# Performance work log

Hardware: AMD Instinct MI355X
Metric: run time of the kernel (lower is better)

Reference implementation:

```python
import jax, jax.numpy as jnp
import numpy as np

NUM_HEADS = 4
INITIAL_VALUE = 1.0
HEADS_RANGE = 3.0


def rotate_every_two(x):
    x1 = x[..., ::2]
    x2 = x[..., 1::2]
    return jnp.stack([-x2, x1], axis=-1).reshape(x.shape)


def theta_shift(x, sin, cos):
    return x * cos + rotate_every_two(x) * sin


def rel_pos_2d(h, w, key_dim):
    # angle: repeat each frequency twice -> length key_dim
    base = 1.0 / 10000.0 ** jnp.linspace(0.0, 1.0, key_dim // 2)
    angle = jnp.repeat(base, 2)
    decay = jnp.log(1.0 - 2.0 ** (-(INITIAL_VALUE + HEADS_RANGE * jnp.arange(NUM_HEADS, dtype=jnp.float32) / NUM_HEADS)))
    idx = jnp.arange(h * w, dtype=jnp.float32)
    sin = jnp.sin(idx[:, None] * angle[None, :]).reshape(h, w, key_dim)
    cos = jnp.cos(idx[:, None] * angle[None, :]).reshape(h, w, key_dim)
    def decay_1d(l):
        i = jnp.arange(l, dtype=jnp.float32)
        return jnp.abs(i[:, None] - i[None, :])[None, :, :] * decay[:, None, None]  # (n, l, l)
    return sin, cos, decay_1d(h), decay_1d(w)


def setup_inputs() -> dict:
    key = jax.random.key(0)
    b, C, H, W = 16, 256, 64, 64
    ks = jax.random.split(key, 12)
    gain = 2.0 ** (-2.5)
    xav = (2.0 / (C + C)) ** 0.5
    return {
        "x": jax.random.normal(ks[0], (b, C, H, W), jnp.float32),
        "Wq": jax.random.normal(ks[1], (C, C), jnp.float32) * gain * xav,
        "bq": jnp.zeros((C,), jnp.float32),
        "Wk": jax.random.normal(ks[2], (C, C), jnp.float32) * gain * xav,
        "bk": jnp.zeros((C,), jnp.float32),
        "Wv": jax.random.normal(ks[3], (C, C), jnp.float32) * gain * xav,
        "bv": jnp.zeros((C,), jnp.float32),
        "dw_kernel": jax.random.normal(ks[4], (5, 5, 1, C), jnp.float32) * 0.05,
        "dw_bias": jnp.zeros((C,), jnp.float32),
        "Wo": jax.random.normal(ks[5], (C, C), jnp.float32) * xav,
        "bo": jnp.zeros((C,), jnp.float32),
    }


def reference(x, Wq, bq, Wk, bk, Wv, bv, dw_kernel, dw_bias, Wo, bo):
    x = jnp.transpose(x, (0, 2, 3, 1))  # (b, h, w, c)
    b, h, w, c = x.shape
    n = NUM_HEADS
    d = c // n  # key_dim == head_dim (value_factor=1)
    scaling = d ** (-0.5)

    sin, cos, mask_h, mask_w = rel_pos_2d(h, w, d)

    q = x @ Wq + bq
    k = (x @ Wk + bk) * scaling
    v = x @ Wv + bv  # (b, h, w, c)

    # depthwise 5x5 conv (lepe) on v, NHWC
    lepe = jax.lax.conv_general_dilated(
        v, dw_kernel, window_strides=(1, 1), padding=((2, 2), (2, 2)),
        dimension_numbers=("NHWC", "HWIO", "NHWC"), feature_group_count=c,
    ) + dw_bias

    q = q.reshape(b, h, w, n, d).transpose(0, 3, 1, 2, 4)  # (b, n, h, w, d)
    k = k.reshape(b, h, w, n, d).transpose(0, 3, 1, 2, 4)
    qr = theta_shift(q, sin, cos)  # sin/cos (h,w,d) broadcast
    kr = theta_shift(k, sin, cos)

    # width-axis attention: rows independent
    qr_w = qr.transpose(0, 2, 1, 3, 4)  # (b, h, n, w, d)
    kr_w = kr.transpose(0, 2, 1, 3, 4)
    v5 = v.reshape(b, h, w, n, d).transpose(0, 1, 3, 2, 4)  # (b, h, n, w, d)
    qk_w = jnp.einsum("bhnqd,bhnkd->bhnqk", qr_w, kr_w) + mask_w  # (b,h,n,w,w)
    v5 = jnp.einsum("bhnqk,bhnkd->bhnqd", jax.nn.softmax(qk_w, axis=-1), v5)

    # height-axis attention: columns independent
    qr_h = qr.transpose(0, 3, 1, 2, 4)  # (b, w, n, h, d)
    kr_h = kr.transpose(0, 3, 1, 2, 4)
    v6 = v5.transpose(0, 3, 2, 1, 4)  # (b, w, n, h, d)
    qk_h = jnp.einsum("bwnqd,bwnkd->bwnqk", qr_h, kr_h) + mask_h  # (b,w,n,h,h)
    out = jnp.einsum("bwnqk,bwnkd->bwnqd", jax.nn.softmax(qk_h, axis=-1), v6)

    out = out.transpose(0, 3, 1, 2, 4).reshape(b, h, w, c)  # (b,h,w,n*d)
    out = (out + lepe) @ Wo + bo
    return jnp.transpose(out, (0, 3, 1, 2))  # (b, c, h, w)
```

## Files before the change

kernel.cpp:

```cpp
#include <hip/hip_runtime.h>
#include <hip/hip_bf16.h>

typedef unsigned short u16;
typedef unsigned int   u32;
typedef __attribute__((ext_vector_type(8))) short bf16x8;
typedef __attribute__((ext_vector_type(4))) float f32x4;

__device__ __forceinline__ float bf2f(u16 u) {
    union { u32 i; float f; } x; x.i = ((u32)u) << 16; return x.f;
}
__device__ __forceinline__ u16 f2bf(float f) {
    union { float f; u32 i; } x; x.f = f;
    u32 i = x.i;
    u32 r = (i + 0x7fffu + ((i >> 16) & 1u)) >> 16;
    return (u16)r;
}

__global__ void k_tables(float2* __restrict__ csT) {
    int id = blockIdx.x * 256 + threadIdx.x;
    int t = id >> 5, i = id & 31;
    double ang = pow(10000.0, -(double)i / 31.0);
    double a = (double)t * ang;
    csT[id] = make_float2((float)cos(a), (float)sin(a));
}

__global__ __launch_bounds__(256) void k_prep_w(
    const float* __restrict__ Wq, const float* __restrict__ Wk,
    const float* __restrict__ Wv, const float* __restrict__ Wo,
    u16* __restrict__ WTq, u16* __restrict__ WTk,
    u16* __restrict__ WTv, u16* __restrict__ WoT)
{
    __shared__ float T[32][33];
    int z = blockIdx.z;
    const float* W = (z == 0) ? Wq : (z == 1) ? Wk : (z == 2) ? Wv : Wo;
    u16* WT        = (z == 0) ? WTq : (z == 1) ? WTk : (z == 2) ? WTv : WoT;
    int n0 = blockIdx.x * 32, k0 = blockIdx.y * 32;
    int tx = threadIdx.x & 31, ty = threadIdx.x >> 5;
#pragma unroll
    for (int i = 0; i < 4; i++)
        T[ty * 4 + i][tx] = W[(k0 + ty * 4 + i) * 256 + n0 + tx];
    __syncthreads();
#pragma unroll
    for (int i = 0; i < 4; i++)
        WT[(n0 + ty * 4 + i) * 256 + k0 + tx] = f2bf(T[tx][ty * 4 + i]);
}

__global__ __launch_bounds__(512, 1) void k_qkv_fused(
    const float* __restrict__ x, const u16* __restrict__ WTall,
    const float* __restrict__ bq, const float* __restrict__ bk,
    const float* __restrict__ bv,
    const float2* __restrict__ csT,
    u16* __restrict__ qr, u16* __restrict__ kr, u16* __restrict__ vO)
{
    __shared__ alignas(16) u16 Alds[128 * 256];
    __shared__ alignas(16) u16 Blds[2][256 * 64];
    __shared__ float2 SL[128 * 32];

    const int tid = threadIdx.x;
    const int t0 = blockIdx.x * 128;
    const int br = tid >> 3, bc = tid & 7;

    bf16x8 breg[4];
#pragma unroll
    for (int p = 0; p < 4; ++p)
        breg[p] = *(const bf16x8*)(WTall + (size_t)(p * 64 + br) * 256 + bc * 8);

    {
        float* Bf = (float*)&Blds[0][0];
        const int b0 = t0 >> 12, sb0 = t0 & 4095;
        const float* xb = x + ((size_t)b0 * 256) * 4096 + sb0;
#pragma unroll
        for (int ch = 0; ch < 2; ++ch) {
#pragma unroll
            for (int p = 0; p < 8; ++p) {
                int it = p * 512 + tid;
                int c = it >> 5, s4 = (it & 31) * 4;
                float4 v4 = *(const float4*)(xb + (size_t)(ch * 128 + c) * 4096 + s4);
                *(float4*)(Bf + c * 128 + s4) = v4;
            }
            __syncthreads();
#pragma unroll
            for (int p = 0; p < 4; ++p) {
                int it = p * 512 + tid;
                int tok = it & 127, ck = it >> 7;
                u16 tmp[8];
#pragma unroll
                for (int j = 0; j < 8; ++j)
                    tmp[j] = f2bf(Bf[(ck * 8 + j) * 128 + tok]);
                int gc = ch * 16 + ck;
                int gcs = (gc & 24) | ((gc & 7) ^ (tok & 7));
                *(bf16x8*)(Alds + tok * 256 + gcs * 8) = *(bf16x8*)tmp;
            }
            __syncthreads();
        }
    }

    {
        const int sb = t0 & 4095;
#pragma unroll
        for (int p = 0; p < 8; ++p) {
            int idx = p * 512 + tid;
            SL[idx] = csT[(size_t)sb * 32 + idx];
        }
    }

    const int lane = tid & 63, w = tid >> 6;
    const int wr = w >> 2, wc = w & 3;
    const int l15 = lane & 15, l4 = lane >> 4, l7 = lane & 7;

#pragma unroll
    for (int mat = 0; mat < 3; ++mat) {
        f32x4 acc[4][4];
#pragma unroll
        for (int mi = 0; mi < 4; ++mi)
#pragma unroll
            for (int ni = 0; ni < 4; ++ni) acc[mi][ni] = (f32x4)0.f;

#pragma unroll
        for (int ks = 0; ks < 4; ++ks) {
            const int s = mat * 4 + ks;
            u16* Bl = &Blds[s & 1][0];
#pragma unroll
            for (int p = 0; p < 4; ++p) {
                int r = p * 64 + br;
                *(bf16x8*)(Bl + r * 64 + (bc ^ (r & 7)) * 8) = breg[p];
            }
            __syncthreads();
            if (s < 11) {
                const int s2 = s + 1;
                const int mat2 = s2 >> 2, ks2 = s2 & 3;
#pragma unroll
                for (int p = 0; p < 4; ++p)
                    breg[p] = *(const bf16x8*)(WTall + (size_t)mat2 * 65536 +
                                (size_t)(p * 64 + br) * 256 + ks2 * 64 + bc * 8);
            }
#pragma unroll
            for (int kk = 0; kk < 2; ++kk) {
                bf16x8 af[4], bfr[4];
#pragma unroll
                for (int mi = 0; mi < 4; ++mi) {
                    int r = wr * 64 + mi * 16 + l15;
                    af[mi] = *(const bf16x8*)(Alds + r * 256 + (ks * 8 + ((kk * 4 + l4) ^ l7)) * 8);
                }
#pragma unroll
                for (int ni = 0; ni < 4; ++ni) {
                    int r = wc * 64 + ni * 16 + l15;
                    bfr[ni] = *(const bf16x8*)(Bl + r * 64 + ((kk * 4 + l4) ^ l7) * 8);
                }
#pragma unroll
                for (int mi = 0; mi < 4; ++mi)
#pragma unroll
                    for (int ni = 0; ni < 4; ++ni)
                        acc[mi][ni] = __builtin_amdgcn_mfma_f32_16x16x32_bf16(
                            af[mi], bfr[ni], acc[mi][ni], 0, 0, 0);
            }
        }

        const float* bias = (mat == 0) ? bq : (mat == 1) ? bk : bv;
        u16* out          = (mat == 0) ? qr : (mat == 1) ? kr : vO;
        const float kscale = (mat == 1) ? 0.125f : 1.0f;
        float bcol[4]; int ip[4];
#pragma unroll
        for (int ni = 0; ni < 4; ++ni) {
            bcol[ni] = bias[wc * 64 + ni * 16 + l15];
            ip[ni] = (ni * 16 + l15) >> 1;
        }
#pragma unroll
        for (int mi = 0; mi < 4; ++mi) {
#pragma unroll
            for (int rg = 0; rg < 4; ++rg) {
                const int sl = wr * 64 + mi * 16 + l4 * 4 + rg;
                size_t trow = (size_t)(t0 + sl) * 256;
#pragma unroll
                for (int ni = 0; ni < 4; ++ni) {
                    float val = (acc[mi][ni][rg] + bcol[ni]) * kscale;
                    float prt = __shfl_xor(val, 1);
                    float res, res2;
                    if (mat != 2) {
                        float2 cs = SL[sl * 32 + ip[ni]];
                        res  = fmaf(val, cs.x, -prt * cs.y);
                        res2 = fmaf(prt, cs.x,  val * cs.y);
                    } else {
                        res = val; res2 = prt;
                    }
                    if (!(lane & 1)) {
                        u32 pk;
                        asm("v_cvt_pk_bf16_f32 %0, %1, %2" : "=v"(pk) : "v"(res), "v"(res2));
                        int o = wc * 64 + ni * 16 + l15;
                        *(u32*)(out + trow + o) = pk;
                    }
                }
            }
        }
    }
}

__global__ __launch_bounds__(256) void k_lepe(
    const u16* __restrict__ v, const float* __restrict__ dwk,
    const float* __restrict__ dwb, u16* __restrict__ lepe)
{
    __shared__ u16 VhU[12 * 12 * 64];
    __shared__ float Kl[25][64];
    const int b = blockIdx.z, cg = blockIdx.y * 64;
    const int ty0 = (blockIdx.x >> 3) * 8, tx0 = (blockIdx.x & 7) * 8;
    const int tid = threadIdx.x;

    for (int idx = tid; idx < 1600; idx += 256) {
        int tap = idx >> 6, c = idx & 63;
        Kl[tap][c] = dwk[tap * 256 + cg + c];
    }
#pragma unroll
    for (int p = 0; p < 9; ++p) {
        int idx = p * 256 + tid;
        int ch = idx & 15, pos = idx >> 4;
        int py = pos / 12, px = pos - py * 12;
        int gy = ty0 + py - 2, gx = tx0 + px - 2;
        ushort4 val = make_ushort4(0, 0, 0, 0);
        if (gy >= 0 && gy < 64 && gx >= 0 && gx < 64)
            val = *(const ushort4*)(v + (size_t)(b * 4096 + gy * 64 + gx) * 256 + cg + ch * 4);
        *(ushort4*)(VhU + pos * 64 + ch * 4) = val;
    }
    __syncthreads();

    const int c = tid & 63, pg = tid >> 6;
    float kreg[25];
#pragma unroll
    for (int t = 0; t < 25; t++) kreg[t] = Kl[t][c];
    const float bias = dwb[cg + c];

    float acc[2][8];
#pragma unroll
    for (int t = 0; t < 2; ++t)
#pragma unroll
        for (int ox = 0; ox < 8; ++ox) acc[t][ox] = bias;

#pragma unroll
    for (int rr = 0; rr < 6; ++rr) {
        const int r = pg * 2 + rr;
        float rv[12];
#pragma unroll
        for (int px = 0; px < 12; ++px)
            rv[px] = bf2f(VhU[(r * 12 + px) * 64 + c]);
        if (rr <= 4) {
            const int dy = rr;
#pragma unroll
            for (int ox = 0; ox < 8; ++ox)
#pragma unroll
                for (int dx = 0; dx < 5; ++dx)
                    acc[0][ox] = fmaf(rv[ox + dx], kreg[dy * 5 + dx], acc[0][ox]);
        }
        if (rr >= 1) {
            const int dy = rr - 1;
#pragma unroll
            for (int ox = 0; ox < 8; ++ox)
#pragma unroll
                for (int dx = 0; dx < 5; ++dx)
                    acc[1][ox] = fmaf(rv[ox + dx], kreg[dy * 5 + dx], acc[1][ox]);
        }
    }

#pragma unroll
    for (int t = 0; t < 2; ++t) {
        const int oy = pg * 2 + t;
#pragma unroll
        for (int ox = 0; ox < 8; ++ox)
            lepe[(size_t)(b * 4096 + (ty0 + oy) * 64 + tx0 + ox) * 256 + cg + c] =
                f2bf(acc[t][ox]);
    }
}

template <int AXIS>
__global__ __launch_bounds__(256) void k_attn_mfma(
    const u16* __restrict__ qr, const u16* __restrict__ kr,
    const u16* __restrict__ vsrc, const u16* __restrict__ lepeP,
    u16* __restrict__ outb)
{
    __shared__ u16 VT[4][64 * 72];
    __shared__ u16 PL[4][64 * 72];

    const int tid = threadIdx.x;
    const int w = tid >> 6, lane = tid & 63;
    const int l15 = lane & 15, l4 = lane >> 4;
    const int wid = blockIdx.x * 4 + w;
    const int b = wid >> 8, xy = (wid >> 2) & 63, n = wid & 3;

    size_t qkbase, vbase; int qkstride, vstride;
    if (AXIS == 0) {
        qkbase = ((size_t)(b * 4096 + xy * 64)) * 256 + n * 64;
        qkstride = 256;
        vbase = qkbase; vstride = 256;
    } else {
        qkbase = ((size_t)(b * 4096 + xy)) * 256 + n * 64;
        qkstride = 64 * 256;
        vbase = ((size_t)((b * 64 + xy) * 4 + n)) * 4096;
        vstride = 64;
    }

    u16* VTl = &VT[w][0];
    u16* PLl = &PL[w][0];

    bf16x8 vld[8];
    const int vrow = lane >> 3, vchunk = lane & 7;
#pragma unroll
    for (int it = 0; it < 8; ++it)
        vld[it] = *(const bf16x8*)(vsrc + vbase + (size_t)(it * 8 + vrow) * vstride + vchunk * 8);

    bf16x8 ka[4][2], qb[4][2];
#pragma unroll
    for (int t = 0; t < 4; ++t)
#pragma unroll
        for (int ks = 0; ks < 2; ++ks) {
            ka[t][ks] = *(const bf16x8*)(kr + qkbase + (size_t)(t * 16 + l15) * qkstride + ks * 32 + l4 * 8);
            qb[t][ks] = *(const bf16x8*)(qr + qkbase + (size_t)(t * 16 + l15) * qkstride + ks * 32 + l4 * 8);
        }

    f32x4 sacc[4][4];
#pragma unroll
    for (int kt = 0; kt < 4; ++kt)
#pragma unroll
        for (int qt = 0; qt < 4; ++qt) sacc[kt][qt] = (f32x4)0.f;
#pragma unroll
    for (int ks = 0; ks < 2; ++ks)
#pragma unroll
        for (int kt = 0; kt < 4; ++kt)
#pragma unroll
            for (int qt = 0; qt < 4; ++qt)
                sacc[kt][qt] = __builtin_amdgcn_mfma_f32_16x16x32_bf16(
                    ka[kt][ks], qb[qt][ks], sacc[kt][qt], 0, 0, 0);

#pragma unroll
    for (int it = 0; it < 8; ++it) {
        int gp = ((it ^ vchunk) << 3) + vrow;
#pragma unroll
        for (int j = 0; j < 8; ++j) {
            int d = vchunk * 8 + j;
            VTl[d * 72 + gp] = (u16)vld[it][j];
        }
    }

    const float decay = logf(1.0f - exp2f(-(1.0f + 0.75f * (float)n)));
#pragma unroll
    for (int qt = 0; qt < 4; ++qt) {
        const int qq = qt * 16 + l15;
        float lsum = 0.f;
#pragma unroll
        for (int kt = 0; kt < 4; ++kt) {
            const int kb = kt * 16 + l4 * 4;
#pragma unroll
            for (int rr = 0; rr < 4; ++rr) {
                float s = sacc[kt][qt][rr] + fabsf((float)(qq - kb - rr)) * decay;
                s = __expf(s);
                sacc[kt][qt][rr] = s;
                lsum += s;
            }
        }
        lsum += __shfl_xor(lsum, 16);
        lsum += __shfl_xor(lsum, 32);
        const float rinv = 1.0f / lsum;
#pragma unroll
        for (int kt = 0; kt < 4; ++kt) {
            float e0 = sacc[kt][qt][0] * rinv, e1 = sacc[kt][qt][1] * rinv;
            float e2 = sacc[kt][qt][2] * rinv, e3 = sacc[kt][qt][3] * rinv;
            u32 p0, p1;
            asm("v_cvt_pk_bf16_f32 %0, %1, %2" : "=v"(p0) : "v"(e0), "v"(e1));
            asm("v_cvt_pk_bf16_f32 %0, %1, %2" : "=v"(p1) : "v"(e2), "v"(e3));
            uint2 pp; pp.x = p0; pp.y = p1;
            *(uint2*)(PLl + (qt * 16 + l15) * 72 + kt * 16 + l4 * 4) = pp;
        }
    }

    __builtin_amdgcn_s_waitcnt(0xC07F);
    bf16x8 pa[4][2], vb[4][2];
#pragma unroll
    for (int qt = 0; qt < 4; ++qt)
#pragma unroll
        for (int ks = 0; ks < 2; ++ks)
            pa[qt][ks] = *(const bf16x8*)(PLl + (qt * 16 + l15) * 72 + ks * 32 + l4 * 8);
#pragma unroll
    for (int dt = 0; dt < 4; ++dt)
#pragma unroll
        for (int ks = 0; ks < 2; ++ks) {
            int d = dt * 16 + l15;
            int g = (ks * 4 + l4) ^ (d >> 3);
            vb[dt][ks] = *(const bf16x8*)(VTl + d * 72 + g * 8);
        }

    f32x4 oacc[4][4];
#pragma unroll
    for (int qt = 0; qt < 4; ++qt)
#pragma unroll
        for (int dt = 0; dt < 4; ++dt) oacc[qt][dt] = (f32x4)0.f;
#pragma unroll
    for (int ks = 0; ks < 2; ++ks)
#pragma unroll
        for (int qt = 0; qt < 4; ++qt)
#pragma unroll
            for (int dt = 0; dt < 4; ++dt)
                oacc[qt][dt] = __builtin_amdgcn_mfma_f32_16x16x32_bf16(
                    pa[qt][ks], vb[dt][ks], oacc[qt][dt], 0, 0, 0);

#pragma unroll
    for (int qt = 0; qt < 4; ++qt)
#pragma unroll
        for (int dt = 0; dt < 4; ++dt)
#pragma unroll
            for (int rr = 0; rr < 4; ++rr)
                PLl[(qt * 16 + l4 * 4 + rr) * 72 + dt * 16 + l15] = f2bf(oacc[qt][dt][rr]);
    __builtin_amdgcn_s_waitcnt(0xC07F);

    size_t orow;
    if (AXIS == 0) orow = ((size_t)((b * 64 + lane) * 4 + n)) * 4096 + xy * 64;
    else           orow = ((size_t)(b * 4096 + lane * 64 + xy)) * 256 + n * 64;
#pragma unroll
    for (int c = 0; c < 8; ++c) {
        bf16x8 o8 = *(const bf16x8*)(PLl + lane * 72 + c * 8);
        if (AXIS == 1) {
            bf16x8 lp = *(const bf16x8*)(lepeP + orow + c * 8);
            u16 hv[8];
#pragma unroll
            for (int j = 0; j < 8; ++j)
                hv[j] = f2bf(bf2f((u16)o8[j]) + bf2f((u16)lp[j]));
            o8 = *(bf16x8*)hv;
        }
        *(bf16x8*)(outb + orow + c * 8) = o8;
    }
}

__global__ __launch_bounds__(512, 1) void k_proj_fused(
    const u16* __restrict__ WoT, const u16* __restrict__ attnL,
    const float* __restrict__ bo, float* __restrict__ y)
{
    __shared__ alignas(16) u16 Alds[128 * 256];
    __shared__ alignas(16) u16 Blds[2][256 * 64];

    const int tid = threadIdx.x;
    const int bid = blockIdx.x;
    const int xcd = bid & 7, slot = bid >> 3;
    const int tt = xcd * 32 + (slot >> 1);
    const int oh = slot & 1;
    const int t0 = tt * 256;
    const int o0 = oh * 128;

    const int ar = tid >> 5, ac = tid & 31;
    const int br = tid >> 3, bc = tid & 7;

    bf16x8 breg[4];
    {
        bf16x8 areg[8];
#pragma unroll
        for (int p = 0; p < 8; ++p)
            areg[p] = *(const bf16x8*)(WoT + (size_t)(o0 + p * 16 + ar) * 256 + ac * 8);
#pragma unroll
        for (int p = 0; p < 4; ++p)
            breg[p] = *(const bf16x8*)(attnL + (size_t)(t0 + p * 64 + br) * 256 + bc * 8);
#pragma unroll
        for (int p = 0; p < 8; ++p) {
            int r = p * 16 + ar;
            *(bf16x8*)(Alds + r * 256 + (ac ^ (r & 7)) * 8) = areg[p];
        }
    }

    const int lane = tid & 63, w = tid >> 6;
    const int wr = w >> 2, wc = w & 3;
    const int l15 = lane & 15, l4 = lane >> 4, l7 = lane & 7;

    f32x4 acc[4][4];
#pragma unroll
    for (int mi = 0; mi < 4; ++mi)
#pragma unroll
        for (int ni = 0; ni < 4; ++ni) acc[mi][ni] = (f32x4)0.f;

#pragma unroll
    for (int ks = 0; ks < 4; ++ks) {
        u16* Bl = &Blds[ks & 1][0];
#pragma unroll
        for (int p = 0; p < 4; ++p) {
            int r = p * 64 + br;
            *(bf16x8*)(Bl + r * 64 + (bc ^ (r & 7)) * 8) = breg[p];
        }
        __syncthreads();
        if (ks < 3) {
#pragma unroll
            for (int p = 0; p < 4; ++p)
                breg[p] = *(const bf16x8*)(attnL + (size_t)(t0 + p * 64 + br) * 256 + (ks + 1) * 64 + bc * 8);
        }
#pragma unroll
        for (int kk = 0; kk < 2; ++kk) {
            bf16x8 af[4], bfr[4];
#pragma unroll
            for (int mi = 0; mi < 4; ++mi) {
                int r = wr * 64 + mi * 16 + l15;
                af[mi] = *(const bf16x8*)(Alds + r * 256 + (ks * 8 + ((kk * 4 + l4) ^ l7)) * 8);
            }
#pragma unroll
            for (int ni = 0; ni < 4; ++ni) {
                int r = wc * 64 + ni * 16 + l15;
                bfr[ni] = *(const bf16x8*)(Bl + r * 64 + ((kk * 4 + l4) ^ l7) * 8);
            }
#pragma unroll
            for (int mi = 0; mi < 4; ++mi)
#pragma unroll
                for (int ni = 0; ni < 4; ++ni)
                    acc[mi][ni] = __builtin_amdgcn_mfma_f32_16x16x32_bf16(
                        af[mi], bfr[ni], acc[mi][ni], 0, 0, 0);
        }
    }

    const int b = t0 >> 12, sb = t0 & 4095;
#pragma unroll
    for (int mi = 0; mi < 4; ++mi) {
#pragma unroll
        for (int rg = 0; rg < 4; ++rg) {
            int o = o0 + wr * 64 + mi * 16 + l4 * 4 + rg;
            float bb = bo[o];
            float* yrow = y + ((size_t)(b * 256 + o)) * 4096 + sb + wc * 64;
#pragma unroll
            for (int ni = 0; ni < 4; ++ni)
                yrow[ni * 16 + l15] = acc[mi][ni][rg] + bb;
        }
    }
}

extern "C" void kernel_launch(void* const* d_in, const int* in_sizes, int n_in,
                              void* d_out, int out_size, void* d_ws, size_t ws_size,
                              hipStream_t stream)
{
    const float* x   = (const float*)d_in[0];
    const float* Wq  = (const float*)d_in[1];
    const float* bq  = (const float*)d_in[2];
    const float* Wk  = (const float*)d_in[3];
    const float* bk  = (const float*)d_in[4];
    const float* Wv  = (const float*)d_in[5];
    const float* bv  = (const float*)d_in[6];
    const float* dwk = (const float*)d_in[7];
    const float* dwb = (const float*)d_in[8];
    const float* Wo  = (const float*)d_in[9];
    const float* bo  = (const float*)d_in[10];
    float* y = (float*)d_out;

    char* ws = (char*)d_ws;
    const size_t MB = 1024 * 1024;
    float2* csT = (float2*)(ws);
    u16* WTq = (u16*)(ws + 1 * MB);
    u16* WTk = WTq + 65536;
    u16* WTv = WTk + 65536;
    u16* WoT = WTv + 65536;
    u16* qr   = (u16*)(ws + 2 * MB);
    u16* kr   = (u16*)(ws + 2 * MB + 32 * MB);
    u16* v    = (u16*)(ws + 2 * MB + 64 * MB);
    u16* lepe = (u16*)(ws + 2 * MB + 96 * MB);
    u16* v5   = (u16*)(ws + 2 * MB + 128 * MB);
    u16* attn = v;

    k_tables<<<dim3(512), dim3(256), 0, stream>>>(csT);
    k_prep_w<<<dim3(8, 8, 4), dim3(256), 0, stream>>>(Wq, Wk, Wv, Wo, WTq, WTk, WTv, WoT);
    k_qkv_fused<<<dim3(512), dim3(512), 0, stream>>>(
        x, WTq, bq, bk, bv, csT, qr, kr, v);
    k_lepe<<<dim3(64, 4, 16), dim3(256), 0, stream>>>(v, dwk, dwb, lepe);
    k_attn_mfma<0><<<dim3(1024), dim3(256), 0, stream>>>(qr, kr, v, nullptr, v5);
    k_attn_mfma<1><<<dim3(1024), dim3(256), 0, stream>>>(qr, kr, v5, lepe, attn);
    k_proj_fused<<<dim3(512), dim3(512), 0, stream>>>(WoT, attn, bo, y);
}
```

Baseline: 196.8 us.

## Fuse width-axis attention into QKV projection kernel epilogue

The width-axis attention is folded into the end of the QKV GEMM kernel. Each block holds the V tile still in registers, writes it transposed to shared memory, reloads q/k rows it just wrote, then runs softmax attention per row and head and writes v5 directly. This drops a kernel launch and a full re-read of V from global memory. In exchange the QKV kernel gets longer and uses more registers, and the q/k reads right after the global writes depend on memory visibility within the block.

After: 195.0 us. About the same (-0.9%).

```diff
diff --git a/kernel.cpp b/kernel.cpp
--- a/kernel.cpp
+++ b/kernel.cpp
@@ -50,11 +50,14 @@
     const float* __restrict__ bq, const float* __restrict__ bk,
     const float* __restrict__ bv,
     const float2* __restrict__ csT,
-    u16* __restrict__ qr, u16* __restrict__ kr, u16* __restrict__ vO)
+    u16* __restrict__ qr, u16* __restrict__ kr, u16* __restrict__ vO,
+    u16* __restrict__ v5)
 {
-    __shared__ alignas(16) u16 Alds[128 * 256];
-    __shared__ alignas(16) u16 Blds[2][256 * 64];
-    __shared__ float2 SL[128 * 32];
+    __shared__ alignas(16) char smem[163840];
+    u16* Alds = (u16*)smem;
+    u16* BldsA[2] = { (u16*)(smem + 65536),
+                      (u16*)(smem + 98304) };
+    float2* SL = (float2*)(smem + 131072);
 
     const int tid = threadIdx.x;
     const int t0 = blockIdx.x * 128;
@@ -66,7 +69,7 @@
         breg[p] = *(const bf16x8*)(WTall + (size_t)(p * 64 + br) * 256 + bc * 8);
 
     {
-        float* Bf = (float*)&Blds[0][0];
+        float* Bf = (float*)(smem + 65536);
         const int b0 = t0 >> 12, sb0 = t0 & 4095;
         const float* xb = x + ((size_t)b0 * 256) * 4096 + sb0;
 #pragma unroll
@@ -108,9 +111,10 @@
     const int wr = w >> 2, wc = w & 3;
     const int l15 = lane & 15, l4 = lane >> 4, l7 = lane & 7;
 
+    f32x4 acc[4][4];
+
 #pragma unroll
     for (int mat = 0; mat < 3; ++mat) {
-        f32x4 acc[4][4];
 #pragma unroll
         for (int mi = 0; mi < 4; ++mi)
 #pragma unroll
@@ -119,7 +123,7 @@
 #pragma unroll
         for (int ks = 0; ks < 4; ++ks) {
             const int s = mat * 4 + ks;
-            u16* Bl = &Blds[s & 1][0];
+            u16* Bl = BldsA[s & 1];
 #pragma unroll
             for (int p = 0; p < 4; ++p) {
                 int r = p * 64 + br;
@@ -193,6 +197,132 @@
             }
         }
     }
+
+    __syncthreads();
+    u16* VTl = (u16*)smem + w * 4608;
+    u16* PLl = (u16*)(smem + 73728) + w * 4608;
+
+    {
+        float bcv[4];
+#pragma unroll
+        for (int ni = 0; ni < 4; ++ni) bcv[ni] = bv[wc * 64 + ni * 16 + l15];
+#pragma unroll
+        for (int mi = 0; mi < 4; ++mi)
+#pragma unroll
+            for (int ni = 0; ni < 4; ++ni) {
+                int d = ni * 16 + l15;
+                int gs = (mi * 2 + (l4 >> 1)) ^ (d >> 3);
+                float e0 = acc[mi][ni][0] + bcv[ni], e1 = acc[mi][ni][1] + bcv[ni];
+                float e2 = acc[mi][ni][2] + bcv[ni], e3 = acc[mi][ni][3] + bcv[ni];
+                u32 p0, p1;
+                asm("v_cvt_pk_bf16_f32 %0, %1, %2" : "=v"(p0) : "v"(e0), "v"(e1));
+                asm("v_cvt_pk_bf16_f32 %0, %1, %2" : "=v"(p1) : "v"(e2), "v"(e3));
+                uint2 pp; pp.x = p0; pp.y = p1;
+                *(uint2*)(VTl + d * 72 + gs * 8 + (l4 & 1) * 4) = pp;
+            }
+    }
+
+    asm volatile("s_waitcnt vmcnt(0)" ::: "memory");
+    const size_t qkb = (size_t)(t0 + wr * 64) * 256 + wc * 64;
+    bf16x8 ka[4][2], qb[4][2];
+#pragma unroll
+    for (int t = 0; t < 4; ++t)
+#pragma unroll
+        for (int ks = 0; ks < 2; ++ks) {
+            ka[t][ks] = *(const bf16x8*)(kr + qkb + (size_t)(t * 16 + l15) * 256 + ks * 32 + l4 * 8);
+            qb[t][ks] = *(const bf16x8*)(qr + qkb + (size_t)(t * 16 + l15) * 256 + ks * 32 + l4 * 8);
+        }
+
+    f32x4 sacc[4][4];
+#pragma unroll
+    for (int kt = 0; kt < 4; ++kt)
+#pragma unroll
+        for (int qt = 0; qt < 4; ++qt) sacc[kt][qt] = (f32x4)0.f;
+#pragma unroll
+    for (int ks = 0; ks < 2; ++ks)
+#pragma unroll
+        for (int kt = 0; kt < 4; ++kt)
+#pragma unroll
+            for (int qt = 0; qt < 4; ++qt)
+                sacc[kt][qt] = __builtin_amdgcn_mfma_f32_16x16x32_bf16(
+                    ka[kt][ks], qb[qt][ks], sacc[kt][qt], 0, 0, 0);
+
+    const float decay = logf(1.0f - exp2f(-(1.0f + 0.75f * (float)wc)));
+#pragma unroll
+    for (int qt = 0; qt < 4; ++qt) {
+        const int qq = qt * 16 + l15;
+        float lsum = 0.f;
+#pragma unroll
+        for (int kt = 0; kt < 4; ++kt) {
+            const int kb = kt * 16 + l4 * 4;
+#pragma unroll
+            for (int rr = 0; rr < 4; ++rr) {
+                float s = sacc[kt][qt][rr] + fabsf((float)(qq - kb - rr)) * decay;
+                s = __expf(s);
+                sacc[kt][qt][rr] = s;
+                lsum += s;
+            }
+        }
+        lsum += __shfl_xor(lsum, 16);
+        lsum += __shfl_xor(lsum, 32);
+        const float rinv = 1.0f / lsum;
+#pragma unroll
+        for (int kt = 0; kt < 4; ++kt) {
+            float e0 = sacc[kt][qt][0] * rinv, e1 = sacc[kt][qt][1] * rinv;
+            float e2 = sacc[kt][qt][2] * rinv, e3 = sacc[kt][qt][3] * rinv;
+            u32 p0, p1;
+            asm("v_cvt_pk_bf16_f32 %0, %1, %2" : "=v"(p0) : "v"(e0), "v"(e1));
+            asm("v_cvt_pk_bf16_f32 %0, %1, %2" : "=v"(p1) : "v"(e2), "v"(e3));
+            uint2 pp; pp.x = p0; pp.y = p1;
+            *(uint2*)(PLl + (qt * 16 + l15) * 72 + kt * 16 + l4 * 4) = pp;
+        }
+    }
+
+    __builtin_amdgcn_s_waitcnt(0xC07F);
+    bf16x8 pa[4][2], vb[4][2];
+#pragma unroll
+    for (int qt = 0; qt < 4; ++qt)
+#pragma unroll
+        for (int ks = 0; ks < 2; ++ks)
+            pa[qt][ks] = *(const bf16x8*)(PLl + (qt * 16 + l15) * 72 + ks * 32 + l4 * 8);
+#pragma unroll
+    for (int dt = 0; dt < 4; ++dt)
+#pragma unroll
+        for (int ks = 0; ks < 2; ++ks) {
+            int d = dt * 16 + l15;
+            int g = (ks * 4 + l4) ^ (d >> 3);
+            vb[dt][ks] = *(const bf16x8*)(VTl + d * 72 + g * 8);
+        }
+
+    f32x4 oacc[4][4];
+#pragma unroll
+    for (int qt = 0; qt < 4; ++qt)
+#pragma unroll
+        for (int dt = 0; dt < 4; ++dt) oacc[qt][dt] = (f32x4)0.f;
+#pragma unroll
+    for (int ks = 0; ks < 2; ++ks)
+#pragma unroll
+        for (int qt = 0; qt < 4; ++qt)
+#pragma unroll
+            for (int dt = 0; dt < 4; ++dt)
+                oacc[qt][dt] = __builtin_amdgcn_mfma_f32_16x16x32_bf16(
+                    pa[qt][ks], vb[dt][ks], oacc[qt][dt], 0, 0, 0);
+
+#pragma unroll
+    for (int qt = 0; qt < 4; ++qt)
+#pragma unroll
+        for (int dt = 0; dt < 4; ++dt)
+#pragma unroll
+            for (int rr = 0; rr < 4; ++rr)
+                PLl[(qt * 16 + l4 * 4 + rr) * 72 + dt * 16 + l15] = f2bf(oacc[qt][dt][rr]);
+    __builtin_amdgcn_s_waitcnt(0xC07F);
+
+    const int b0 = t0 >> 12;
+    const int line = ((t0 & 4095) >> 6) + wr;
+    size_t orow = ((size_t)((b0 * 64 + lane) * 4 + wc)) * 4096 + line * 64;
+#pragma unroll
+    for (int c = 0; c < 8; ++c)
+        *(bf16x8*)(v5 + orow + c * 8) = *(const bf16x8*)(PLl + lane * 72 + c * 8);
 }
 
 __global__ __launch_bounds__(256) void k_lepe(
@@ -269,8 +399,7 @@
     }
 }
 
-template <int AXIS>
-__global__ __launch_bounds__(256) void k_attn_mfma(
+__global__ __launch_bounds__(256) void k_attn_h(
     const u16* __restrict__ qr, const u16* __restrict__ kr,
     const u16* __restrict__ vsrc, const u16* __restrict__ lepeP,
     u16* __restrict__ outb)
@@ -284,17 +413,10 @@
     const int wid = blockIdx.x * 4 + w;
     const int b = wid >> 8, xy = (wid >> 2) & 63, n = wid & 3;
 
-    size_t qkbase, vbase; int qkstride, vstride;
-    if (AXIS == 0) {
-        qkbase = ((size_t)(b * 4096 + xy * 64)) * 256 + n * 64;
-        qkstride = 256;
-        vbase = qkbase; vstride = 256;
-    } else {
-        qkbase = ((size_t)(b * 4096 + xy)) * 256 + n * 64;
-        qkstride = 64 * 256;
-        vbase = ((size_t)((b * 64 + xy) * 4 + n)) * 4096;
-        vstride = 64;
-    }
+    const size_t qkbase = ((size_t)(b * 4096 + xy)) * 256 + n * 64;
+    const int qkstride = 64 * 256;
+    const size_t vbase = ((size_t)((b * 64 + xy) * 4 + n)) * 4096;
+    const int vstride = 64;
 
     u16* VTl = &VT[w][0];
     u16* PLl = &PL[w][0];
@@ -408,21 +530,16 @@
                 PLl[(qt * 16 + l4 * 4 + rr) * 72 + dt * 16 + l15] = f2bf(oacc[qt][dt][rr]);
     __builtin_amdgcn_s_waitcnt(0xC07F);
 
-    size_t orow;
-    if (AXIS == 0) orow = ((size_t)((b * 64 + lane) * 4 + n)) * 4096 + xy * 64;
-    else           orow = ((size_t)(b * 4096 + lane * 64 + xy)) * 256 + n * 64;
+    size_t orow = ((size_t)(b * 4096 + lane * 64 + xy)) * 256 + n * 64;
 #pragma unroll
     for (int c = 0; c < 8; ++c) {
         bf16x8 o8 = *(const bf16x8*)(PLl + lane * 72 + c * 8);
-        if (AXIS == 1) {
-            bf16x8 lp = *(const bf16x8*)(lepeP + orow + c * 8);
-            u16 hv[8];
-#pragma unroll
-            for (int j = 0; j < 8; ++j)
-                hv[j] = f2bf(bf2f((u16)o8[j]) + bf2f((u16)lp[j]));
-            o8 = *(bf16x8*)hv;
-        }
-        *(bf16x8*)(outb + orow + c * 8) = o8;
+        bf16x8 lp = *(const bf16x8*)(lepeP + orow + c * 8);
+        u16 hv[8];
+#pragma unroll
+        for (int j = 0; j < 8; ++j)
+            hv[j] = f2bf(bf2f((u16)o8[j]) + bf2f((u16)lp[j]));
+        *(bf16x8*)(outb + orow + c * 8) = *(bf16x8*)hv;
     }
 }
 
@@ -555,9 +672,8 @@
     k_tables<<<dim3(512), dim3(256), 0, stream>>>(csT);
     k_prep_w<<<dim3(8, 8, 4), dim3(256), 0, stream>>>(Wq, Wk, Wv, Wo, WTq, WTk, WTv, WoT);
     k_qkv_fused<<<dim3(512), dim3(512), 0, stream>>>(
-        x, WTq, bq, bk, bv, csT, qr, kr, v);
+        x, WTq, bq, bk, bv, csT, qr, kr, v, v5);
     k_lepe<<<dim3(64, 4, 16), dim3(256), 0, stream>>>(v, dwk, dwb, lepe);
-    k_attn_mfma<0><<<dim3(1024), dim3(256), 0, stream>>>(qr, kr, v, nullptr, v5);
-    k_attn_mfma<1><<<dim3(1024), dim3(256), 0, stream>>>(qr, kr, v5, lepe, attn);
+    k_attn_h<<<dim3(1024), dim3(256), 0, stream>>>(qr, kr, v5, lepe, attn);
     k_proj_fused<<<dim3(512), dim3(512), 0, stream>>>(WoT, attn, bo, y);
 }
```
